# Optimization experiments

Hardware: AMD Instinct MI355X
Metric: run time of the kernel (lower is better)

## Reference

```python
import jax, jax.numpy as jnp
import numpy as np

N = 100000   # nodes
E = 5000000  # edges (avg degree 50)
H = 16       # hidden dim


def gcn_conv(x, edge_index, edge_weight, W, b, num_nodes):
    """PyG GCNConv with edge weights: add self-loops (weight 1), symmetric
    normalization deg^-1/2 * w * deg^-1/2, linear transform, scatter-add."""
    row, col = edge_index[0], edge_index[1]  # source j -> target i
    loop = jnp.arange(num_nodes, dtype=edge_index.dtype)
    row = jnp.concatenate([row, loop])
    col = jnp.concatenate([col, loop])
    w = jnp.concatenate([edge_weight, jnp.ones((num_nodes,), edge_weight.dtype)])
    deg = jax.ops.segment_sum(w, col, num_segments=num_nodes)
    dinv = jnp.where(deg > 0, jax.lax.rsqrt(jnp.where(deg > 0, deg, 1.0)), 0.0)
    norm = dinv[row] * w * dinv[col]               # [E+N]
    h = x @ W                                      # [N, out]
    msg = norm[:, None] * h[row]                   # gather + scale
    out = jax.ops.segment_sum(msg, col, num_segments=num_nodes)  # scatter-add
    return out + b


def setup_inputs() -> dict:
    key = jax.random.key(0)
    k = jax.random.split(key, 7)
    x = jax.random.normal(k[0], (N, 1), dtype=jnp.float32)
    edge_index = jax.random.randint(k[1], (2, E), 0, N, dtype=jnp.int32)
    edge_attr = jax.random.uniform(k[2], (E,), dtype=jnp.float32)
    W1 = jax.random.normal(k[3], (1, H), dtype=jnp.float32) * (1.0 / np.sqrt(1.0))
    b1 = jnp.zeros((H,), dtype=jnp.float32)
    W2 = jax.random.normal(k[4], (H, 1), dtype=jnp.float32) * (1.0 / np.sqrt(H))
    b2 = jnp.zeros((1,), dtype=jnp.float32)
    return {"x": x, "edge_index": edge_index, "edge_attr": edge_attr,
            "W1": W1, "b1": b1, "W2": W2, "b2": b2}


def reference(x, edge_index, edge_attr, W1, b1, W2, b2):
    h = gcn_conv(x, edge_index, edge_attr, W1, b1, N)
    h = jax.nn.relu(h)
    out = gcn_conv(h, edge_index, edge_attr, W2, b2, N)
    return out
```

## Files before the change

### kernel.cpp

```cpp
#include <hip/hip_runtime.h>

#define T       256
#define BSHIFT  12
#define BSIZE   4096
#define MAXNB   32
#define M       32
#define EPB     2048
#define EPT     (EPB / T)

__global__ void k_count(const int* __restrict__ col, int* __restrict__ cntT,
                        int E, int nb, int ebp) {
    __shared__ int hist[MAXNB];
    int t = threadIdx.x, g = blockIdx.x;
    if (t < MAXNB) hist[t] = 0;
    __syncthreads();
    int base = g * EPB;
    bool full = (base + EPB <= E);
    if (full) {
#pragma unroll
        for (int k = 0; k < EPT / 4; ++k) {
            int4 c = *(const int4*)(col + base + (t + k * T) * 4);
            atomicAdd(&hist[c.x >> BSHIFT], 1);
            atomicAdd(&hist[c.y >> BSHIFT], 1);
            atomicAdd(&hist[c.z >> BSHIFT], 1);
            atomicAdd(&hist[c.w >> BSHIFT], 1);
        }
    } else {
        for (int k = 0; k < EPT; ++k) {
            int e = base + t + k * T;
            if (e < E) atomicAdd(&hist[col[e] >> BSHIFT], 1);
        }
    }
    __syncthreads();
    if (t < nb) cntT[t * ebp + g] = hist[t];
}

__global__ void k_scan(const int* __restrict__ cntT, int* __restrict__ ofsT,
                       int* __restrict__ tot, int eb, int ebp) {
    __shared__ int tsum[T];
    __shared__ int carry;
    int b = blockIdx.x, t = threadIdx.x;
    if (t == 0) carry = 0;
    __syncthreads();
    int rounds = (eb + T - 1) / T;
    for (int jr = 0; jr < rounds; ++jr) {
        int idx = jr * T + t;
        int v = (idx < eb) ? cntT[b * ebp + idx] : 0;
        tsum[t] = v;
        __syncthreads();
        for (int d = 1; d < T; d <<= 1) {
            int o = (t >= d) ? tsum[t - d] : 0;
            __syncthreads();
            tsum[t] += o;
            __syncthreads();
        }
        int excl = tsum[t] - v + carry;
        if (idx < eb) ofsT[b * ebp + idx] = excl;
        __syncthreads();
        if (t == 0) carry += tsum[T - 1];
        __syncthreads();
    }
    if (t == 0) tot[b] = carry;
}

__global__ void k_scatter(const int* __restrict__ row, const int* __restrict__ col,
                          const float* __restrict__ w,
                          const int* __restrict__ cntT, const int* __restrict__ ofsT,
                          const int* __restrict__ tot,
                          int2* __restrict__ rec, int E, int nb, int ebp) {
    __shared__ int  lofs[MAXNB + 1];
    __shared__ int  rnk[MAXNB];
    __shared__ int  rbase[MAXNB];
    __shared__ int2 buf[EPB];
    __shared__ unsigned char bkt[EPB];
    int t = threadIdx.x, g = blockIdx.x;
    if (t < MAXNB) rnk[t] = 0;
    if (t < 64) {
        int tv = (t < nb) ? ((tot[t] + 3) & ~3) : 0;
        int incA = tv;
#pragma unroll
        for (int d = 1; d < 32; d <<= 1) {
            int o = __shfl_up(incA, d, 64);
            if (t >= d) incA += o;
        }
        int h = (t < nb) ? cntT[t * ebp + g] : 0;
        int incB = h;
#pragma unroll
        for (int d = 1; d < 32; d <<= 1) {
            int o = __shfl_up(incB, d, 64);
            if (t >= d) incB += o;
        }
        if (t == 0) lofs[0] = 0;
        if (t < nb) {
            lofs[t + 1] = incB;
            rbase[t] = (incA - tv) + ofsT[t * ebp + g];
        }
    }
    __syncthreads();

    int base = g * EPB;
    bool full = (base + EPB <= E);
    if (full) {
#pragma unroll
        for (int k = 0; k < EPT / 4; ++k) {
            int idx = base + (t + k * T) * 4;
            int4   c  = *(const int4*)(col + idx);
            int4   r  = *(const int4*)(row + idx);
            float4 wv = *(const float4*)(w + idx);
            int b, rk, pos;
            b = c.x >> BSHIFT; rk = atomicAdd(&rnk[b], 1); pos = lofs[b] + rk;
            buf[pos] = make_int2(((c.x & (BSIZE-1)) << 17) | r.x, __float_as_int(wv.x));
            bkt[pos] = (unsigned char)b;
            b = c.y >> BSHIFT; rk = atomicAdd(&rnk[b], 1); pos = lofs[b] + rk;
            buf[pos] = make_int2(((c.y & (BSIZE-1)) << 17) | r.y, __float_as_int(wv.y));
            bkt[pos] = (unsigned char)b;
            b = c.z >> BSHIFT; rk = atomicAdd(&rnk[b], 1); pos = lofs[b] + rk;
            buf[pos] = make_int2(((c.z & (BSIZE-1)) << 17) | r.z, __float_as_int(wv.z));
            bkt[pos] = (unsigned char)b;
            b = c.w >> BSHIFT; rk = atomicAdd(&rnk[b], 1); pos = lofs[b] + rk;
            buf[pos] = make_int2(((c.w & (BSIZE-1)) << 17) | r.w, __float_as_int(wv.w));
            bkt[pos] = (unsigned char)b;
        }
    } else {
        for (int k = 0; k < EPT; ++k) {
            int e = base + t + k * T;
            if (e < E) {
                int c = col[e];
                int b = c >> BSHIFT;
                int rk = atomicAdd(&rnk[b], 1);
                int pos = lofs[b] + rk;
                buf[pos] = make_int2(((c & (BSIZE-1)) << 17) | row[e], __float_as_int(w[e]));
                bkt[pos] = (unsigned char)b;
            }
        }
    }
    __syncthreads();
    int total = lofs[nb];
    for (int j = t; j < total; j += T) {
        int b = bkt[j];
        rec[rbase[b] + (j - lofs[b])] = buf[j];
    }
}

template <bool HAS_SRC>
__global__ void k_acc(const int2* __restrict__ rec, const int* __restrict__ tot,
                      const float* __restrict__ src, float* __restrict__ part, int nb) {
    __shared__ float acc[BSIZE];
    __shared__ int   bst[MAXNB];
    int t = threadIdx.x, g = blockIdx.x;
    int b = g / M, m = g % M;
    if (t < 64) {
        int tv = (t < nb) ? ((tot[t] + 3) & ~3) : 0;
        int inc = tv;
#pragma unroll
        for (int d = 1; d < 32; d <<= 1) {
            int o = __shfl_up(inc, d, 64);
            if (t >= d) inc += o;
        }
        if (t < nb) bst[t] = inc - tv;
    }
    for (int j = t; j < BSIZE; j += T) acc[j] = 0.0f;
    __syncthreads();
    int s  = bst[b];
    int tb = tot[b];
    int chunk = ((tb + M - 1) / M + 7) & ~7;
    int lo = s + m * chunk;
    int hi = min(s + tb, lo + chunk);
    const int4* rec4 = (const int4*)rec;
    int i = lo + t * 8;
    for (; i + 7 < hi; i += T * 8) {
        int4 q0 = rec4[(i >> 1) + 0];
        int4 q1 = rec4[(i >> 1) + 1];
        int4 q2 = rec4[(i >> 1) + 2];
        int4 q3 = rec4[(i >> 1) + 3];
        float v0 = __int_as_float(q0.y), v1 = __int_as_float(q0.w);
        float v2 = __int_as_float(q1.y), v3 = __int_as_float(q1.w);
        float v4 = __int_as_float(q2.y), v5 = __int_as_float(q2.w);
        float v6 = __int_as_float(q3.y), v7 = __int_as_float(q3.w);
        if (HAS_SRC) {
            v0 *= src[q0.x & 0x1FFFF]; v1 *= src[q0.z & 0x1FFFF];
            v2 *= src[q1.x & 0x1FFFF]; v3 *= src[q1.z & 0x1FFFF];
            v4 *= src[q2.x & 0x1FFFF]; v5 *= src[q2.z & 0x1FFFF];
            v6 *= src[q3.x & 0x1FFFF]; v7 *= src[q3.z & 0x1FFFF];
        }
        atomicAdd(&acc[((unsigned)q0.x) >> 17], v0);
        atomicAdd(&acc[((unsigned)q0.z) >> 17], v1);
        atomicAdd(&acc[((unsigned)q1.x) >> 17], v2);
        atomicAdd(&acc[((unsigned)q1.z) >> 17], v3);
        atomicAdd(&acc[((unsigned)q2.x) >> 17], v4);
        atomicAdd(&acc[((unsigned)q2.z) >> 17], v5);
        atomicAdd(&acc[((unsigned)q3.x) >> 17], v6);
        atomicAdd(&acc[((unsigned)q3.z) >> 17], v7);
    }
    for (; i < hi; ++i) {
        int2 r = rec[i];
        float v = __int_as_float(r.y);
        if (HAS_SRC) v *= src[r.x & 0x1FFFF];
        atomicAdd(&acc[((unsigned)r.x) >> 17], v);
    }
    __syncthreads();
    float* dst = part + (size_t)g * BSIZE;
    for (int j = t; j < BSIZE; j += T) dst[j] = acc[j];
}

__device__ __forceinline__ float reduceM(const float* __restrict__ part, int n) {
    int b = n >> BSHIFT, o = n & (BSIZE - 1);
    const float* pp = part + (size_t)b * M * BSIZE + o;
    float s = 0.0f;
#pragma unroll
    for (int m = 0; m < M; ++m) s += pp[(size_t)m * BSIZE];
    return s;
}

__global__ void k_red_dinv(const float* __restrict__ part, const float* __restrict__ x,
                           float* __restrict__ dinv, float* __restrict__ p, int N) {
    int i = blockIdx.x * blockDim.x + threadIdx.x;
    if (i < N) {
        float d  = reduceM(part, i) + 1.0f;
        float di = rsqrtf(d);
        dinv[i] = di;
        p[i] = di * x[i];
    }
}

__global__ void k_red_mlp(const float* __restrict__ part, const float* __restrict__ dinv,
                          const float* __restrict__ p,
                          const float* __restrict__ W1, const float* __restrict__ b1,
                          const float* __restrict__ W2,
                          float* __restrict__ q, int N) {
    int i = blockIdx.x * blockDim.x + threadIdx.x;
    if (i < N) {
        float di = dinv[i];
        float s  = di * reduceM(part, i) + di * p[i];
        float acc = 0.0f;
#pragma unroll
        for (int k = 0; k < 16; ++k) {
            float h = fmaxf(s * W1[k] + b1[k], 0.0f);
            acc += h * W2[k];
        }
        q[i] = di * acc;
    }
}

__global__ void k_red_out(const float* __restrict__ part, const float* __restrict__ dinv,
                          const float* __restrict__ q, const float* __restrict__ b2,
                          float* __restrict__ out, int N) {
    int i = blockIdx.x * blockDim.x + threadIdx.x;
    if (i < N) {
        float di = dinv[i];
        out[i] = di * reduceM(part, i) + di * q[i] + b2[0];
    }
}

extern "C" void kernel_launch(void* const* d_in, const int* in_sizes, int n_in,
                              void* d_out, int out_size, void* d_ws, size_t ws_size,
                              hipStream_t stream) {
    const float* x  = (const float*)d_in[0];
    const int*   ei = (const int*)  d_in[1];
    const float* ew = (const float*)d_in[2];
    const float* W1 = (const float*)d_in[3];
    const float* b1 = (const float*)d_in[4];
    const float* W2 = (const float*)d_in[5];
    const float* b2 = (const float*)d_in[6];

    const int N = in_sizes[0];
    const int E = in_sizes[2];
    const int* row = ei;
    const int* col = ei + E;
    const int nb  = (N + BSIZE - 1) >> BSHIFT;
    const int eb  = (E + EPB - 1) / EPB;
    const int ebp = (eb + 63) & ~63;

    char* wsp = (char*)d_ws;
    auto take = [&](size_t bytes) {
        char* r = wsp; wsp += (bytes + 255) & ~(size_t)255; return (void*)r;
    };
    int2*  rec  = (int2*) take((size_t)(E + 4 * MAXNB) * 8);
    float* part = (float*)take((size_t)nb * M * BSIZE * 4);
    float* dinv = (float*)take((size_t)N * 4);
    float* p    = (float*)take((size_t)N * 4);
    float* q    = (float*)take((size_t)N * 4);
    int*   cntT = (int*)  take((size_t)MAXNB * ebp * 4);
    int*   ofsT = (int*)  take((size_t)MAXNB * ebp * 4);
    int*   tot  = (int*)  take(MAXNB * 4);

    float* out = (float*)d_out;

    const int nbk = (N + T - 1) / T;
    const int ab  = nb * M;

    k_count  <<<eb, T, 0, stream>>>(col, cntT, E, nb, ebp);
    k_scan   <<<nb, T, 0, stream>>>(cntT, ofsT, tot, eb, ebp);
    k_scatter<<<eb, T, 0, stream>>>(row, col, ew, cntT, ofsT, tot, rec, E, nb, ebp);

    k_acc<false><<<ab, T, 0, stream>>>(rec, tot, nullptr, part, nb);
    k_red_dinv  <<<nbk, T, 0, stream>>>(part, x, dinv, p, N);

    k_acc<true><<<ab, T, 0, stream>>>(rec, tot, p, part, nb);
    k_red_mlp  <<<nbk, T, 0, stream>>>(part, dinv, p, W1, b1, W2, q, N);

    k_acc<true><<<ab, T, 0, stream>>>(rec, tot, q, part, nb);
    k_red_out  <<<nbk, T, 0, stream>>>(part, dinv, q, b2, out, N);
}
```

Before: 240.2 us.

## Bin edges into 2D (destination, source) tiles to stage source values in LDS

Edges are now bucketed by both destination block and source block, giving 625 cells of 4096x4096 instead of 25 destination blocks split across 32 slices. Each accumulation block handles one cell and loads its 4096-entry source slice into shared memory, so the gather of per-node source values reads LDS instead of random global memory. The count and scatter histograms grow to up to 640 bins and scatter now recomputes its own histogram. Edges per block double to 4096. Costs: more scan blocks, a larger partial buffer (625x4096 floats), and a reduction loop over 25 partials per node.

Measured after the change: 317.2 us. 32.1% more time.

```diff
diff --git a/kernel.cpp b/kernel.cpp
--- a/kernel.cpp
+++ b/kernel.cpp
@@ -1,51 +1,50 @@
 #include <hip/hip_runtime.h>
 
 #define T       256
-#define BSHIFT  12
-#define BSIZE   4096
-#define MAXNB   32
-#define M       32
-#define EPB     2048
+#define BSH     12
+#define BS      4096
+#define MAXC    640
+#define EPB     4096
 #define EPT     (EPB / T)
 
-__global__ void k_count(const int* __restrict__ col, int* __restrict__ cntT,
-                        int E, int nb, int ebp) {
-    __shared__ int hist[MAXNB];
+__global__ void k_count(const int* __restrict__ col, const int* __restrict__ row,
+                        int* __restrict__ cntT, int E, int nbr, int ncell, int ebp) {
+    __shared__ int hist[MAXC];
     int t = threadIdx.x, g = blockIdx.x;
-    if (t < MAXNB) hist[t] = 0;
+    for (int j = t; j < ncell; j += T) hist[j] = 0;
     __syncthreads();
     int base = g * EPB;
-    bool full = (base + EPB <= E);
-    if (full) {
+    int hiE  = min(E, base + EPB);
+    if (base + EPB <= E) {
+        const int4* col4 = (const int4*)(col + base);
+        const int4* row4 = (const int4*)(row + base);
 #pragma unroll
         for (int k = 0; k < EPT / 4; ++k) {
-            int4 c = *(const int4*)(col + base + (t + k * T) * 4);
-            atomicAdd(&hist[c.x >> BSHIFT], 1);
-            atomicAdd(&hist[c.y >> BSHIFT], 1);
-            atomicAdd(&hist[c.z >> BSHIFT], 1);
-            atomicAdd(&hist[c.w >> BSHIFT], 1);
+            int4 c = col4[t + k * T];
+            int4 r = row4[t + k * T];
+            atomicAdd(&hist[(c.x >> BSH) * nbr + (r.x >> BSH)], 1);
+            atomicAdd(&hist[(c.y >> BSH) * nbr + (r.y >> BSH)], 1);
+            atomicAdd(&hist[(c.z >> BSH) * nbr + (r.z >> BSH)], 1);
+            atomicAdd(&hist[(c.w >> BSH) * nbr + (r.w >> BSH)], 1);
         }
     } else {
-        for (int k = 0; k < EPT; ++k) {
-            int e = base + t + k * T;
-            if (e < E) atomicAdd(&hist[col[e] >> BSHIFT], 1);
-        }
-    }
-    __syncthreads();
-    if (t < nb) cntT[t * ebp + g] = hist[t];
-}
-
-__global__ void k_scan(const int* __restrict__ cntT, int* __restrict__ ofsT,
-                       int* __restrict__ tot, int eb, int ebp) {
+        for (int e = base + t; e < hiE; e += T)
+            atomicAdd(&hist[(col[e] >> BSH) * nbr + (row[e] >> BSH)], 1);
+    }
+    __syncthreads();
+    for (int j = t; j < ncell; j += T) cntT[(size_t)j * ebp + g] = hist[j];
+}
+
+__global__ void k_scan(int* __restrict__ cntT, int* __restrict__ tot, int eb, int ebp) {
     __shared__ int tsum[T];
     __shared__ int carry;
-    int b = blockIdx.x, t = threadIdx.x;
+    int c = blockIdx.x, t = threadIdx.x;
     if (t == 0) carry = 0;
     __syncthreads();
     int rounds = (eb + T - 1) / T;
     for (int jr = 0; jr < rounds; ++jr) {
         int idx = jr * T + t;
-        int v = (idx < eb) ? cntT[b * ebp + idx] : 0;
+        int v = (idx < eb) ? cntT[(size_t)c * ebp + idx] : 0;
         tsum[t] = v;
         __syncthreads();
         for (int d = 1; d < T; d <<= 1) {
@@ -55,88 +54,103 @@
             __syncthreads();
         }
         int excl = tsum[t] - v + carry;
-        if (idx < eb) ofsT[b * ebp + idx] = excl;
+        if (idx < eb) cntT[(size_t)c * ebp + idx] = excl;
         __syncthreads();
         if (t == 0) carry += tsum[T - 1];
         __syncthreads();
     }
-    if (t == 0) tot[b] = carry;
+    if (t == 0) tot[c] = carry;
 }
 
 __global__ void k_scatter(const int* __restrict__ row, const int* __restrict__ col,
                           const float* __restrict__ w,
-                          const int* __restrict__ cntT, const int* __restrict__ ofsT,
+                          const int* __restrict__ ofsT,
                           const int* __restrict__ tot,
-                          int2* __restrict__ rec, int E, int nb, int ebp) {
-    __shared__ int  lofs[MAXNB + 1];
-    __shared__ int  rnk[MAXNB];
-    __shared__ int  rbase[MAXNB];
+                          int2* __restrict__ rec, int E, int nbr, int ncell, int ebp) {
     __shared__ int2 buf[EPB];
-    __shared__ unsigned char bkt[EPB];
+    __shared__ unsigned short bkt[EPB];
+    __shared__ int hist[MAXC], rnk[MAXC], lofs[MAXC], rbase[MAXC];
     int t = threadIdx.x, g = blockIdx.x;
-    if (t < MAXNB) rnk[t] = 0;
+    for (int j = t; j < ncell; j += T) { hist[j] = 0; rnk[j] = 0; }
+    __syncthreads();
+    int base = g * EPB;
+    int hiE  = min(E, base + EPB);
+    bool full = (base + EPB <= E);
+
+    if (full) {
+        const int4* col4 = (const int4*)(col + base);
+        const int4* row4 = (const int4*)(row + base);
+#pragma unroll
+        for (int k = 0; k < EPT / 4; ++k) {
+            int4 c = col4[t + k * T];
+            int4 r = row4[t + k * T];
+            atomicAdd(&hist[(c.x >> BSH) * nbr + (r.x >> BSH)], 1);
+            atomicAdd(&hist[(c.y >> BSH) * nbr + (r.y >> BSH)], 1);
+            atomicAdd(&hist[(c.z >> BSH) * nbr + (r.z >> BSH)], 1);
+            atomicAdd(&hist[(c.w >> BSH) * nbr + (r.w >> BSH)], 1);
+        }
+    } else {
+        for (int e = base + t; e < hiE; e += T)
+            atomicAdd(&hist[(col[e] >> BSH) * nbr + (row[e] >> BSH)], 1);
+    }
+    __syncthreads();
+
     if (t < 64) {
-        int tv = (t < nb) ? ((tot[t] + 3) & ~3) : 0;
-        int incA = tv;
-#pragma unroll
-        for (int d = 1; d < 32; d <<= 1) {
-            int o = __shfl_up(incA, d, 64);
-            if (t >= d) incA += o;
-        }
-        int h = (t < nb) ? cntT[t * ebp + g] : 0;
-        int incB = h;
-#pragma unroll
-        for (int d = 1; d < 32; d <<= 1) {
-            int o = __shfl_up(incB, d, 64);
-            if (t >= d) incB += o;
-        }
-        if (t == 0) lofs[0] = 0;
-        if (t < nb) {
-            lofs[t + 1] = incB;
-            rbase[t] = (incA - tv) + ofsT[t * ebp + g];
-        }
-    }
-    __syncthreads();
-
-    int base = g * EPB;
-    bool full = (base + EPB <= E);
+        int carryA = 0, carryB = 0;
+        for (int ch = 0; ch * 64 < ncell; ++ch) {
+            int i = ch * 64 + t;
+            int tv = (i < ncell) ? ((tot[i] + 7) & ~7) : 0;
+            int hv = (i < ncell) ? hist[i] : 0;
+            int ia = tv, ib = hv;
+#pragma unroll
+            for (int d = 1; d < 64; d <<= 1) {
+                int oa = __shfl_up(ia, d, 64);
+                int ob = __shfl_up(ib, d, 64);
+                if (t >= d) { ia += oa; ib += ob; }
+            }
+            if (i < ncell) {
+                lofs[i]  = ib - hv + carryB;
+                rbase[i] = (ia - tv + carryA) + ofsT[(size_t)i * ebp + g];
+            }
+            carryA += __shfl(ia, 63, 64);
+            carryB += __shfl(ib, 63, 64);
+        }
+    }
+    __syncthreads();
+
     if (full) {
+        const int4*   col4 = (const int4*)(col + base);
+        const int4*   row4 = (const int4*)(row + base);
+        const float4* w4   = (const float4*)(w + base);
 #pragma unroll
         for (int k = 0; k < EPT / 4; ++k) {
-            int idx = base + (t + k * T) * 4;
-            int4   c  = *(const int4*)(col + idx);
-            int4   r  = *(const int4*)(row + idx);
-            float4 wv = *(const float4*)(w + idx);
+            int4 c = col4[t + k * T];
+            int4 r = row4[t + k * T];
+            float4 wv = w4[t + k * T];
             int b, rk, pos;
-            b = c.x >> BSHIFT; rk = atomicAdd(&rnk[b], 1); pos = lofs[b] + rk;
-            buf[pos] = make_int2(((c.x & (BSIZE-1)) << 17) | r.x, __float_as_int(wv.x));
-            bkt[pos] = (unsigned char)b;
-            b = c.y >> BSHIFT; rk = atomicAdd(&rnk[b], 1); pos = lofs[b] + rk;
-            buf[pos] = make_int2(((c.y & (BSIZE-1)) << 17) | r.y, __float_as_int(wv.y));
-            bkt[pos] = (unsigned char)b;
-            b = c.z >> BSHIFT; rk = atomicAdd(&rnk[b], 1); pos = lofs[b] + rk;
-            buf[pos] = make_int2(((c.z & (BSIZE-1)) << 17) | r.z, __float_as_int(wv.z));
-            bkt[pos] = (unsigned char)b;
-            b = c.w >> BSHIFT; rk = atomicAdd(&rnk[b], 1); pos = lofs[b] + rk;
-            buf[pos] = make_int2(((c.w & (BSIZE-1)) << 17) | r.w, __float_as_int(wv.w));
-            bkt[pos] = (unsigned char)b;
+            b = (c.x >> BSH) * nbr + (r.x >> BSH); rk = atomicAdd(&rnk[b], 1); pos = lofs[b] + rk;
+            buf[pos] = make_int2(((c.x & (BS-1)) << 17) | r.x, __float_as_int(wv.x)); bkt[pos] = (unsigned short)b;
+            b = (c.y >> BSH) * nbr + (r.y >> BSH); rk = atomicAdd(&rnk[b], 1); pos = lofs[b] + rk;
+            buf[pos] = make_int2(((c.y & (BS-1)) << 17) | r.y, __float_as_int(wv.y)); bkt[pos] = (unsigned short)b;
+            b = (c.z >> BSH) * nbr + (r.z >> BSH); rk = atomicAdd(&rnk[b], 1); pos = lofs[b] + rk;
+            buf[pos] = make_int2(((c.z & (BS-1)) << 17) | r.z, __float_as_int(wv.z)); bkt[pos] = (unsigned short)b;
+            b = (c.w >> BSH) * nbr + (r.w >> BSH); rk = atomicAdd(&rnk[b], 1); pos = lofs[b] + rk;
+            buf[pos] = make_int2(((c.w & (BS-1)) << 17) | r.w, __float_as_int(wv.w)); bkt[pos] = (unsigned short)b;
         }
     } else {
-        for (int k = 0; k < EPT; ++k) {
-            int e = base + t + k * T;
-            if (e < E) {
-                int c = col[e];
-                int b = c >> BSHIFT;
-                int rk = atomicAdd(&rnk[b], 1);
-                int pos = lofs[b] + rk;
-                buf[pos] = make_int2(((c & (BSIZE-1)) << 17) | row[e], __float_as_int(w[e]));
-                bkt[pos] = (unsigned char)b;
-            }
-        }
-    }
-    __syncthreads();
-    int total = lofs[nb];
-    for (int j = t; j < total; j += T) {
+        for (int e = base + t; e < hiE; e += T) {
+            int cc = col[e], rr = row[e];
+            int b = (cc >> BSH) * nbr + (rr >> BSH);
+            int rk = atomicAdd(&rnk[b], 1);
+            int pos = lofs[b] + rk;
+            buf[pos] = make_int2(((cc & (BS-1)) << 17) | rr, __float_as_int(w[e]));
+            bkt[pos] = (unsigned short)b;
+        }
+    }
+    __syncthreads();
+
+    int totalT = hiE - base;
+    for (int j = t; j < totalT; j += T) {
         int b = bkt[j];
         rec[rbase[b] + (j - lofs[b])] = buf[j];
     }
@@ -144,28 +158,34 @@
 
 template <bool HAS_SRC>
 __global__ void k_acc(const int2* __restrict__ rec, const int* __restrict__ tot,
-                      const float* __restrict__ src, float* __restrict__ part, int nb) {
-    __shared__ float acc[BSIZE];
-    __shared__ int   bst[MAXNB];
-    int t = threadIdx.x, g = blockIdx.x;
-    int b = g / M, m = g % M;
+                      const float* __restrict__ src, float* __restrict__ part,
+                      int N, int nbr, int ncell) {
+    __shared__ float acc[BS];
+    __shared__ float srcl[BS];
+    __shared__ int sBase;
+    int t = threadIdx.x, c = blockIdx.x;
     if (t < 64) {
-        int tv = (t < nb) ? ((tot[t] + 3) & ~3) : 0;
-        int inc = tv;
-#pragma unroll
-        for (int d = 1; d < 32; d <<= 1) {
-            int o = __shfl_up(inc, d, 64);
-            if (t >= d) inc += o;
-        }
-        if (t < nb) bst[t] = inc - tv;
-    }
-    for (int j = t; j < BSIZE; j += T) acc[j] = 0.0f;
-    __syncthreads();
-    int s  = bst[b];
-    int tb = tot[b];
-    int chunk = ((tb + M - 1) / M + 7) & ~7;
-    int lo = s + m * chunk;
-    int hi = min(s + tb, lo + chunk);
+        int s = 0;
+        for (int ch = 0; ch * 64 < c; ++ch) {
+            int i = ch * 64 + t;
+            if (i < c) s += (tot[i] + 7) & ~7;
+        }
+#pragma unroll
+        for (int d = 1; d < 64; d <<= 1) s += __shfl_xor(s, d, 64);
+        if (t == 0) sBase = s;
+    }
+    for (int j = t; j < BS; j += T) acc[j] = 0.0f;
+    if (HAS_SRC) {
+        int rb = c % nbr;
+        int base = rb << BSH;
+        for (int j = t; j < BS; j += T) {
+            int gg = base + j;
+            srcl[j] = (gg < N) ? src[gg] : 0.0f;
+        }
+    }
+    __syncthreads();
+    int lo = sBase;
+    int hi = lo + tot[c];
     const int4* rec4 = (const int4*)rec;
     int i = lo + t * 8;
     for (; i + 7 < hi; i += T * 8) {
@@ -178,10 +198,10 @@
         float v4 = __int_as_float(q2.y), v5 = __int_as_float(q2.w);
         float v6 = __int_as_float(q3.y), v7 = __int_as_float(q3.w);
         if (HAS_SRC) {
-            v0 *= src[q0.x & 0x1FFFF]; v1 *= src[q0.z & 0x1FFFF];
-            v2 *= src[q1.x & 0x1FFFF]; v3 *= src[q1.z & 0x1FFFF];
-            v4 *= src[q2.x & 0x1FFFF]; v5 *= src[q2.z & 0x1FFFF];
-            v6 *= src[q3.x & 0x1FFFF]; v7 *= src[q3.z & 0x1FFFF];
+            v0 *= srcl[q0.x & (BS-1)]; v1 *= srcl[q0.z & (BS-1)];
+            v2 *= srcl[q1.x & (BS-1)]; v3 *= srcl[q1.z & (BS-1)];
+            v4 *= srcl[q2.x & (BS-1)]; v5 *= srcl[q2.z & (BS-1)];
+            v6 *= srcl[q3.x & (BS-1)]; v7 *= srcl[q3.z & (BS-1)];
         }
         atomicAdd(&acc[((unsigned)q0.x) >> 17], v0);
         atomicAdd(&acc[((unsigned)q0.z) >> 17], v1);
@@ -195,28 +215,27 @@
     for (; i < hi; ++i) {
         int2 r = rec[i];
         float v = __int_as_float(r.y);
-        if (HAS_SRC) v *= src[r.x & 0x1FFFF];
+        if (HAS_SRC) v *= srcl[r.x & (BS-1)];
         atomicAdd(&acc[((unsigned)r.x) >> 17], v);
     }
     __syncthreads();
-    float* dst = part + (size_t)g * BSIZE;
-    for (int j = t; j < BSIZE; j += T) dst[j] = acc[j];
-}
-
-__device__ __forceinline__ float reduceM(const float* __restrict__ part, int n) {
-    int b = n >> BSHIFT, o = n & (BSIZE - 1);
-    const float* pp = part + (size_t)b * M * BSIZE + o;
+    float* dst = part + (size_t)c * BS;
+    for (int j = t; j < BS; j += T) dst[j] = acc[j];
+}
+
+__device__ __forceinline__ float reduceM(const float* __restrict__ part, int n, int nbr) {
+    int b = n >> BSH, o = n & (BS - 1);
+    const float* pp = part + (size_t)b * nbr * BS + o;
     float s = 0.0f;
-#pragma unroll
-    for (int m = 0; m < M; ++m) s += pp[(size_t)m * BSIZE];
+    for (int m = 0; m < nbr; ++m) s += pp[(size_t)m * BS];
     return s;
 }
 
 __global__ void k_red_dinv(const float* __restrict__ part, const float* __restrict__ x,
-                           float* __restrict__ dinv, float* __restrict__ p, int N) {
+                           float* __restrict__ dinv, float* __restrict__ p, int N, int nbr) {
     int i = blockIdx.x * blockDim.x + threadIdx.x;
     if (i < N) {
-        float d  = reduceM(part, i) + 1.0f;
+        float d  = reduceM(part, i, nbr) + 1.0f;
         float di = rsqrtf(d);
         dinv[i] = di;
         p[i] = di * x[i];
@@ -227,11 +246,11 @@
                           const float* __restrict__ p,
                           const float* __restrict__ W1, const float* __restrict__ b1,
                           const float* __restrict__ W2,
-                          float* __restrict__ q, int N) {
+                          float* __restrict__ q, int N, int nbr) {
     int i = blockIdx.x * blockDim.x + threadIdx.x;
     if (i < N) {
         float di = dinv[i];
-        float s  = di * reduceM(part, i) + di * p[i];
+        float s  = di * reduceM(part, i, nbr) + di * p[i];
         float acc = 0.0f;
 #pragma unroll
         for (int k = 0; k < 16; ++k) {
@@ -244,11 +263,11 @@
 
 __global__ void k_red_out(const float* __restrict__ part, const float* __restrict__ dinv,
                           const float* __restrict__ q, const float* __restrict__ b2,
-                          float* __restrict__ out, int N) {
+                          float* __restrict__ out, int N, int nbr) {
     int i = blockIdx.x * blockDim.x + threadIdx.x;
     if (i < N) {
         float di = dinv[i];
-        out[i] = di * reduceM(part, i) + di * q[i] + b2[0];
+        out[i] = di * reduceM(part, i, nbr) + di * q[i] + b2[0];
     }
 }
 
@@ -267,38 +286,38 @@
     const int E = in_sizes[2];
     const int* row = ei;
     const int* col = ei + E;
-    const int nb  = (N + BSIZE - 1) >> BSHIFT;
-    const int eb  = (E + EPB - 1) / EPB;
-    const int ebp = (eb + 63) & ~63;
+    const int nbc   = (N + BS - 1) >> BSH;
+    const int nbr   = nbc;
+    const int ncell = nbc * nbr;
+    const int eb    = (E + EPB - 1) / EPB;
+    const int ebp   = (eb + 63) & ~63;
 
     char* wsp = (char*)d_ws;
     auto take = [&](size_t bytes) {
         char* r = wsp; wsp += (bytes + 255) & ~(size_t)255; return (void*)r;
     };
-    int2*  rec  = (int2*) take((size_t)(E + 4 * MAXNB) * 8);
-    float* part = (float*)take((size_t)nb * M * BSIZE * 4);
+    int2*  rec  = (int2*) take((size_t)(E + 8 * MAXC) * 8);
+    float* part = (float*)take((size_t)ncell * BS * 4);
+    int*   cntT = (int*)  take((size_t)ncell * ebp * 4);
+    int*   tot  = (int*)  take(MAXC * 4);
     float* dinv = (float*)take((size_t)N * 4);
     float* p    = (float*)take((size_t)N * 4);
     float* q    = (float*)take((size_t)N * 4);
-    int*   cntT = (int*)  take((size_t)MAXNB * ebp * 4);
-    int*   ofsT = (int*)  take((size_t)MAXNB * ebp * 4);
-    int*   tot  = (int*)  take(MAXNB * 4);
 
     float* out = (float*)d_out;
 
     const int nbk = (N + T - 1) / T;
-    const int ab  = nb * M;
-
-    k_count  <<<eb, T, 0, stream>>>(col, cntT, E, nb, ebp);
-    k_scan   <<<nb, T, 0, stream>>>(cntT, ofsT, tot, eb, ebp);
-    k_scatter<<<eb, T, 0, stream>>>(row, col, ew, cntT, ofsT, tot, rec, E, nb, ebp);
-
-    k_acc<false><<<ab, T, 0, stream>>>(rec, tot, nullptr, part, nb);
-    k_red_dinv  <<<nbk, T, 0, stream>>>(part, x, dinv, p, N);
-
-    k_acc<true><<<ab, T, 0, stream>>>(rec, tot, p, part, nb);
-    k_red_mlp  <<<nbk, T, 0, stream>>>(part, dinv, p, W1, b1, W2, q, N);
-
-    k_acc<true><<<ab, T, 0, stream>>>(rec, tot, q, part, nb);
-    k_red_out  <<<nbk, T, 0, stream>>>(part, dinv, q, b2, out, N);
-}
+
+    k_count  <<<eb, T, 0, stream>>>(col, row, cntT, E, nbr, ncell, ebp);
+    k_scan   <<<ncell, T, 0, stream>>>(cntT, tot, eb, ebp);
+    k_scatter<<<eb, T, 0, stream>>>(row, col, ew, cntT, tot, rec, E, nbr, ncell, ebp);
+
+    k_acc<false><<<ncell, T, 0, stream>>>(rec, tot, nullptr, part, N, nbr, ncell);
+    k_red_dinv  <<<nbk, T, 0, stream>>>(part, x, dinv, p, N, nbr);
+
+    k_acc<true><<<ncell, T, 0, stream>>>(rec, tot, p, part, N, nbr, ncell);
+    k_red_mlp  <<<nbk, T, 0, stream>>>(part, dinv, p, W1, b1, W2, q, N, nbr);
+
+    k_acc<true><<<ncell, T, 0, stream>>>(rec, tot, q, part, N, nbr, ncell);
+    k_red_out  <<<nbk, T, 0, stream>>>(part, dinv, q, b2, out, N, nbr);
+}
```
